# Kernel tuning notes

Hardware: AMD Instinct MI355X
Metric: run time of the kernel (lower is better)

## Reference

```python
import jax, jax.numpy as jnp
import numpy as np
import math

B, N, M, C, H = 4, 2048, 2048, 512, 4
D_V = C // H          # 128, used for scale and value head dim
D_QK = 2 * C // H     # 256, q/k head dim due to seq-axis split of the 2*dim qkv output
SCALE = D_V ** -0.5
EPS = 1e-12           # F.normalize eps


def _l2norm(t):
    n = jnp.linalg.norm(t, axis=-1, keepdims=True)
    return t / jnp.maximum(n, EPS)


def setup_inputs() -> dict:
    key = jax.random.key(0)
    k1, k2, k3, k4 = jax.random.split(key, 4)
    x = jax.random.normal(k1, (B, N, C), dtype=jnp.float32)
    context = jax.random.normal(k2, (B, M, C), dtype=jnp.float32)
    W_qkv = jax.random.normal(k3, (2 * C, C), dtype=jnp.float32) * 0.02  # torch Linear weight [out,in]
    W_proj = jax.random.normal(k4, (C, C), dtype=jnp.float32) * 0.02
    radius = jnp.ones((H,), dtype=jnp.float32) * math.sqrt(D_V)
    return {"x": x, "context": context, "W_qkv": W_qkv, "W_proj": W_proj, "radius": radius}


def reference(x, context, W_qkv, W_proj, radius):
    # qkv(cat([x, context], dim=1)) then split along sequence: q from x rows, k from context rows
    q = jnp.einsum('bnc,oc->bno', x, W_qkv)        # [B,N,2C]
    k = jnp.einsum('bmc,oc->bmo', context, W_qkv)  # [B,M,2C]
    q = q.reshape(B, N, H, D_QK).transpose(0, 2, 1, 3)       # [B,H,N,256]
    k = k.reshape(B, M, H, D_QK).transpose(0, 2, 1, 3)       # [B,H,M,256]
    v = context.reshape(B, M, H, D_V).transpose(0, 2, 1, 3)  # [B,H,M,128]
    r = radius[None, :, None, None]
    q = _l2norm(q) * r
    k = _l2norm(k) * r
    attn = jnp.einsum('bhnd,bhmd->bhnm', q, k) * SCALE
    attn = jax.nn.softmax(attn, axis=-1)
    out = jnp.einsum('bhnm,bhmd->bhnd', attn, v)
    out = out.transpose(0, 2, 1, 3).reshape(B, N, C)
    return jnp.einsum('bnc,oc->bno', out, W_proj)
```

## Files before the change

kernel.cpp:

```cpp
#include <hip/hip_runtime.h>
#include <hip/hip_bf16.h>
#include <stdint.h>

#define SCALE_F 0.08838834764831845f
#define LOG2E_F 1.4426950408889634f

typedef __attribute__((ext_vector_type(8))) short short8;
typedef __attribute__((ext_vector_type(4))) float f32x4;
typedef __attribute__((ext_vector_type(16))) float f32x16;
typedef __attribute__((ext_vector_type(2))) unsigned int uint2v;

__device__ __forceinline__ void g2l16(const void* g, void* l) {
  __builtin_amdgcn_global_load_lds(
      (const __attribute__((address_space(1))) void*)g,
      (__attribute__((address_space(3))) void*)l, 16, 0, 0);
}

__device__ __forceinline__ unsigned pkbf(float a, float b) {
  union { __hip_bfloat16 h[2]; unsigned u; } o;
  o.h[0] = __float2bfloat16(a); o.h[1] = __float2bfloat16(b);
  return o.u;
}

__global__ __launch_bounds__(256) void convert_all(
    const float* __restrict__ x, const float* __restrict__ wqkv,
    const float* __restrict__ wproj,
    __hip_bfloat16* __restrict__ ab, __hip_bfloat16* __restrict__ wb,
    __hip_bfloat16* __restrict__ wpb)
{
  size_t qi = (size_t)blockIdx.x * 256 + threadIdx.x;
  const float* src; __hip_bfloat16* dst; size_t off;
  if (qi < 1048576)      { src = x;     dst = ab;  off = qi; }
  else if (qi < 1179648) { src = wqkv;  dst = wb;  off = qi - 1048576; }
  else                   { src = wproj; dst = wpb; off = qi - 1179648; }
  float4 v = ((const float4*)src)[off];
  union { __hip_bfloat16 h4[4]; uint2 u; } o;
  o.h4[0] = __float2bfloat16(v.x); o.h4[1] = __float2bfloat16(v.y);
  o.h4[2] = __float2bfloat16(v.z); o.h4[3] = __float2bfloat16(v.w);
  ((uint2*)dst)[off] = o.u;
}

__global__ __launch_bounds__(256) void transpose_v(
    const float* __restrict__ ctx, __hip_bfloat16* __restrict__ vt,
    __hip_bfloat16* __restrict__ abctx)
{
  __shared__ float tile[128][33];
  const int bid = blockIdx.x;
  const int mt = bid & 63;
  const int bh = bid >> 6;
  const int h = bh & 3, b = bh >> 2;
  const int tid = threadIdx.x;
  for (int i = 0; i < 16; ++i) {
    int idx = i * 256 + tid;
    int mm = idx >> 7, d = idx & 127;
    tile[d][mm] = ctx[((size_t)b * 2048 + mt * 32 + mm) * 512 + h * 128 + d];
  }
  __syncthreads();
  for (int i = 0; i < 16; ++i) {
    int idx = i * 256 + tid;
    int d = idx >> 5, mm = idx & 31;
    vt[((size_t)bh * 128 + d) * 2048 + mt * 32 + mm] = __float2bfloat16(tile[d][mm]);
  }
  for (int i = 0; i < 16; ++i) {
    int idx = i * 256 + tid;
    int mm = idx >> 7, d = idx & 127;
    abctx[((size_t)b * 2048 + mt * 32 + mm) * 512 + h * 128 + d] =
        __float2bfloat16(tile[d][mm]);
  }
}

__global__ __launch_bounds__(256) void gemm_qkv(
    const __hip_bfloat16* __restrict__ A,
    const __hip_bfloat16* __restrict__ Bw,
    const float* __restrict__ radius,
    __hip_bfloat16* __restrict__ qn, __hip_bfloat16* __restrict__ kn)
{
  __shared__ __hip_bfloat16 sAB[384 * 32];
  __hip_bfloat16* sA = sAB;
  __hip_bfloat16* sB = sAB + 64 * 32;
  const int tid = threadIdx.x;
  const int wave = tid >> 6, lane = tid & 63;
  const int ln = lane & 15, q4 = lane >> 4;
  const int ro = blockIdx.x >> 2;
  const int co = blockIdx.x & 3;
  const __hip_bfloat16* Ab = A + (size_t)ro * 64 * 512;
  const __hip_bfloat16* Bb = Bw + (size_t)co * 256 * 512;
  const int row0 = tid >> 2, p0 = tid & 3;
  f32x4 acc[16] = {};
  for (int k0 = 0; k0 < 512; k0 += 32) {
    g2l16(Ab + (size_t)row0 * 512 + k0 + p0 * 8, (char*)sA + tid * 16);
#pragma unroll
    for (int i = 0; i < 4; ++i)
      g2l16(Bb + (size_t)(i * 64 + row0) * 512 + k0 + p0 * 8,
            (char*)sB + (i * 256 + tid) * 16);
    __syncthreads();
    short8 af = *(const short8*)(sA + (wave * 16 + ln) * 32 + q4 * 8);
#pragma unroll
    for (int ni = 0; ni < 16; ++ni) {
      short8 bf = *(const short8*)(sB + (ni * 16 + ln) * 32 + q4 * 8);
      acc[ni] = __builtin_amdgcn_mfma_f32_16x16x32_bf16(af, bf, acc[ni], 0, 0, 0);
    }
    __syncthreads();
  }
  const float rad = radius[co];
  const int grow0 = ro * 64;
  const bool isq = grow0 < 8192;
  const int rl = isq ? grow0 : grow0 - 8192;
  const float qfac = isq ? rad * rad * SCALE_F * LOG2E_F : 1.0f;
  float scl[4];
#pragma unroll
  for (int r = 0; r < 4; ++r) {
    float ss = 0.f;
#pragma unroll
    for (int ni = 0; ni < 16; ++ni) { float v = acc[ni][r]; ss += v * v; }
    ss += __shfl_xor(ss, 1); ss += __shfl_xor(ss, 2);
    ss += __shfl_xor(ss, 4); ss += __shfl_xor(ss, 8);
    scl[r] = qfac / fmaxf(sqrtf(ss), 1e-12f);
  }
  __hip_bfloat16* dstT = (isq ? qn : kn) +
      ((size_t)((rl >> 11) * 4 + co) * 2048 + (rl & 2047)) * 256;
  __hip_bfloat16* sEw = sAB + wave * 3072;
#pragma unroll
  for (int c = 0; c < 2; ++c) {
    if ((q4 >> 1) == c) {
      int lr = (q4 & 1) * 4;
#pragma unroll
      for (int r = 0; r < 4; ++r)
#pragma unroll
        for (int ni = 0; ni < 16; ++ni)
          sEw[(lr + r) * 264 + ni * 16 + ln] =
              __float2bfloat16(acc[ni][r] * scl[r]);
    }
    asm volatile("s_waitcnt lgkmcnt(0)" ::: "memory");
#pragma unroll
    for (int p = 0; p < 4; ++p) {
      int idx = p * 64 + lane;
      int rr = idx >> 5, c8 = idx & 31;
      short8 v = *(const short8*)(sEw + rr * 264 + c8 * 8);
      *(short8*)(dstT + (size_t)(wave * 16 + c * 8 + rr) * 256 + c8 * 8) = v;
    }
    asm volatile("s_waitcnt lgkmcnt(0)" ::: "memory");
  }
}

__global__ __launch_bounds__(256) void gemm_nt(
    const __hip_bfloat16* __restrict__ A, const __hip_bfloat16* __restrict__ B,
    float* __restrict__ C, int O, int K, int tiles_o)
{
  __shared__ __hip_bfloat16 sA[128 * 32];
  __shared__ __hip_bfloat16 sB[128 * 32];
  const int tid = threadIdx.x;
  const int wave = tid >> 6, lane = tid & 63;
  const int ln = lane & 15, q = lane >> 4;
  const int br = (blockIdx.x / tiles_o) * 128;
  const int bo = (blockIdx.x % tiles_o) * 128;
  const int wr = (wave >> 1) * 64, wc = (wave & 1) * 64;
  const __hip_bfloat16* Ab = A + (size_t)br * K;
  const __hip_bfloat16* Bb = B + (size_t)bo * K;
  const int row0 = tid >> 2, p0 = tid & 3;
  f32x4 acc[4][4] = {};
  for (int k0 = 0; k0 < K; k0 += 32) {
    for (int i = 0; i < 2; ++i) {
      int row = i * 64 + row0;
      g2l16(Ab + (size_t)row * K + k0 + p0 * 8, (char*)sA + (i * 256 + tid) * 16);
      g2l16(Bb + (size_t)row * K + k0 + p0 * 8, (char*)sB + (i * 256 + tid) * 16);
    }
    __syncthreads();
    short8 af[4], bfr[4];
    for (int mi = 0; mi < 4; ++mi)
      af[mi] = *(const short8*)(sA + (wr + mi * 16 + ln) * 32 + q * 8);
    for (int ni = 0; ni < 4; ++ni)
      bfr[ni] = *(const short8*)(sB + (wc + ni * 16 + ln) * 32 + q * 8);
    for (int mi = 0; mi < 4; ++mi)
      for (int ni = 0; ni < 4; ++ni)
        acc[mi][ni] = __builtin_amdgcn_mfma_f32_16x16x32_bf16(af[mi], bfr[ni], acc[mi][ni], 0, 0, 0);
    __syncthreads();
  }
  for (int mi = 0; mi < 4; ++mi)
    for (int ni = 0; ni < 4; ++ni) {
      int rg = br + wr + mi * 16 + q * 4;
      int cg = bo + wc + ni * 16 + ln;
      for (int r = 0; r < 4; ++r)
        C[(size_t)(rg + r) * O + cg] = acc[mi][ni][r];
    }
}

__global__ __launch_bounds__(256, 2) void attn(
    const __hip_bfloat16* __restrict__ qn,
    const __hip_bfloat16* __restrict__ kn,
    const __hip_bfloat16* __restrict__ vt,
    float* __restrict__ Op,
    float* __restrict__ den)
{
  __shared__ __hip_bfloat16 sK[2][32 * 256];
  __shared__ __hip_bfloat16 sV[2][128 * 32];
  const int tid = threadIdx.x, wave = tid >> 6, lane = tid & 63;
  const int m32 = lane & 31, hi = lane >> 5;
  const int i = blockIdx.x;
  const int bh = (i & 7) + 8 * ((i >> 3) & 1);
  const int half = (i >> 4) & 1;
  const int nt = i >> 5;
  const int mbase = half * 1024;
  const __hip_bfloat16* Q = qn + ((size_t)bh * 2048 + nt * 128 + wave * 32) * 256;
  const __hip_bfloat16* Kp = kn + (size_t)bh * 2048 * 256;
  const __hip_bfloat16* Vp = vt + (size_t)bh * 128 * 2048;

  short8 qf[16];
  for (int kk = 0; kk < 16; ++kk)
    qf[kk] = *(const short8*)(Q + m32 * 256 + kk * 16 + hi * 8);

  f32x16 oacc[4];
  for (int v = 0; v < 4; ++v)
    for (int j = 0; j < 16; ++j) oacc[v][j] = 0.f;
  float denom = 0.f;

  for (int t = 0; t < 4; ++t) {
    int D = t * 256 + tid, row = D >> 5, cc = D & 31;
    g2l16(Kp + (size_t)(mbase + row) * 256 + ((cc ^ (row & 7)) << 3),
          (char*)sK[0] + D * 16);
  }
  for (int t = 0; t < 2; ++t) {
    int D = t * 256 + tid, rd = D >> 2, cc = D & 3;
    g2l16(Vp + (size_t)rd * 2048 + mbase + ((cc ^ ((rd >> 1) & 3)) << 3),
          (char*)sV[0] + D * 16);
  }
  __syncthreads();

  for (int it = 0; it < 32; ++it) {
    const int cur = it & 1, nxt = cur ^ 1;
    if (it + 1 < 32) {
      const int m1 = mbase + (it + 1) * 32;
      for (int t = 0; t < 4; ++t) {
        int D = t * 256 + tid, row = D >> 5, cc = D & 31;
        g2l16(Kp + (size_t)(m1 + row) * 256 + ((cc ^ (row & 7)) << 3),
              (char*)sK[nxt] + D * 16);
      }
      for (int t = 0; t < 2; ++t) {
        int D = t * 256 + tid, rd = D >> 2, cc = D & 3;
        g2l16(Vp + (size_t)rd * 2048 + m1 + ((cc ^ ((rd >> 1) & 3)) << 3),
              (char*)sV[nxt] + D * 16);
      }
    }
    const __hip_bfloat16* sKc = sK[cur];
    f32x16 sa, sb;
    for (int j = 0; j < 16; ++j) { sa[j] = 0.f; sb[j] = 0.f; }
#pragma unroll
    for (int kk = 0; kk < 8; ++kk) {
      int ca = kk * 2 + hi, cb = (kk + 8) * 2 + hi;
      short8 kfa = *(const short8*)(sKc + m32 * 256 + ((ca ^ (m32 & 7)) << 3));
      short8 kfb = *(const short8*)(sKc + m32 * 256 + ((cb ^ (m32 & 7)) << 3));
      sa = __builtin_amdgcn_mfma_f32_32x32x16_bf16(kfa, qf[kk], sa, 0, 0, 0);
      sb = __builtin_amdgcn_mfma_f32_32x32x16_bf16(kfb, qf[kk + 8], sb, 0, 0, 0);
    }
    union { unsigned u[4]; short8 s; } ua, ub;
    {
      float e0, e1, e2, e3;
      unsigned u0, u1, u2, u3;
      e0 = __builtin_exp2f(sa[0] + sb[0]); e1 = __builtin_exp2f(sa[1] + sb[1]);
      e2 = __builtin_exp2f(sa[2] + sb[2]); e3 = __builtin_exp2f(sa[3] + sb[3]);
      denom += (e0 + e1) + (e2 + e3);
      u0 = pkbf(e0, e1); u1 = pkbf(e2, e3);
      e0 = __builtin_exp2f(sa[4] + sb[4]); e1 = __builtin_exp2f(sa[5] + sb[5]);
      e2 = __builtin_exp2f(sa[6] + sb[6]); e3 = __builtin_exp2f(sa[7] + sb[7]);
      denom += (e0 + e1) + (e2 + e3);
      u2 = pkbf(e0, e1); u3 = pkbf(e2, e3);
      uint2v s0 = __builtin_amdgcn_permlane32_swap(u0, u2, false, false);
      uint2v s1 = __builtin_amdgcn_permlane32_swap(u1, u3, false, false);
      ua.u[0] = s0.x; ua.u[1] = s1.x; ua.u[2] = s0.y; ua.u[3] = s1.y;
      e0 = __builtin_exp2f(sa[8] + sb[8]);   e1 = __builtin_exp2f(sa[9] + sb[9]);
      e2 = __builtin_exp2f(sa[10] + sb[10]); e3 = __builtin_exp2f(sa[11] + sb[11]);
      denom += (e0 + e1) + (e2 + e3);
      u0 = pkbf(e0, e1); u1 = pkbf(e2, e3);
      e0 = __builtin_exp2f(sa[12] + sb[12]); e1 = __builtin_exp2f(sa[13] + sb[13]);
      e2 = __builtin_exp2f(sa[14] + sb[14]); e3 = __builtin_exp2f(sa[15] + sb[15]);
      denom += (e0 + e1) + (e2 + e3);
      u2 = pkbf(e0, e1); u3 = pkbf(e2, e3);
      uint2v s2 = __builtin_amdgcn_permlane32_swap(u0, u2, false, false);
      uint2v s3 = __builtin_amdgcn_permlane32_swap(u1, u3, false, false);
      ub.u[0] = s2.x; ub.u[1] = s3.x; ub.u[2] = s2.y; ub.u[3] = s3.y;
    }
    const __hip_bfloat16* sVc = sV[cur];
#pragma unroll
    for (int kc = 0; kc < 2; ++kc) {
      short8 pf = kc ? ub.s : ua.s;
#pragma unroll
      for (int vi = 0; vi < 4; ++vi) {
        int rd = vi * 32 + m32;
        int c = kc * 2 + hi;
        short8 vf = *(const short8*)(sVc + rd * 32 + ((c ^ ((rd >> 1) & 3)) << 3));
        oacc[vi] = __builtin_amdgcn_mfma_f32_32x32x16_bf16(vf, pf, oacc[vi], 0, 0, 0);
      }
    }
    __syncthreads();
  }

  float dfull = denom + __shfl_xor(denom, 32);
  float* Opb = Op + (size_t)(half * 16 + bh) * 2048 * 128;
  float* denb = den + (size_t)(half * 16 + bh) * 2048;
  const int rbase = nt * 128 + wave * 32;
  if (hi == 0) denb[rbase + m32] = dfull;
  float* sc_ = (float*)(&sK[0][0]) + wave * 1056;
#pragma unroll
  for (int vi = 0; vi < 4; ++vi) {
#pragma unroll
    for (int reg = 0; reg < 16; ++reg) {
      int dL = (reg & 3) + 8 * (reg >> 2) + 4 * hi;
      sc_[m32 * 33 + dL] = oacc[vi][reg];
    }
    asm volatile("s_waitcnt lgkmcnt(0)" ::: "memory");
#pragma unroll
    for (int qq = 0; qq < 16; ++qq) {
      int qr = qq * 2 + hi;
      Opb[(size_t)(rbase + qr) * 128 + vi * 32 + m32] = sc_[qr * 33 + m32];
    }
    asm volatile("s_waitcnt lgkmcnt(0)" ::: "memory");
  }
}

__global__ __launch_bounds__(256) void combine(
    const float* __restrict__ Op, const float* __restrict__ den,
    __hip_bfloat16* __restrict__ ob)
{
  int qi = blockIdx.x * 256 + threadIdx.x;
  int r = qi >> 5;
  int dq = qi & 31;
  int bh = r >> 11, n = r & 2047, b = bh >> 2, h = bh & 3;
  float4 o0 = ((const float4*)Op)[qi];
  float4 o1 = ((const float4*)(Op + 4194304))[qi];
  float inv = 1.0f / (den[r] + den[32768 + r]);
  union { __hip_bfloat16 h4[4]; uint2 u; } o;
  o.h4[0] = __float2bfloat16((o0.x + o1.x) * inv);
  o.h4[1] = __float2bfloat16((o0.y + o1.y) * inv);
  o.h4[2] = __float2bfloat16((o0.z + o1.z) * inv);
  o.h4[3] = __float2bfloat16((o0.w + o1.w) * inv);
  *(uint2*)&ob[((size_t)b * 2048 + n) * 512 + h * 128 + dq * 4] = o.u;
}

extern "C" void kernel_launch(void* const* d_in, const int* in_sizes, int n_in,
                              void* d_out, int out_size, void* d_ws, size_t ws_size,
                              hipStream_t stream) {
  const float* x      = (const float*)d_in[0];
  const float* ctx    = (const float*)d_in[1];
  const float* wqkv   = (const float*)d_in[2];
  const float* wproj  = (const float*)d_in[3];
  const float* radius = (const float*)d_in[4];
  char* ws = (char*)d_ws;
  __hip_bfloat16* ab  = (__hip_bfloat16*)(ws);
  __hip_bfloat16* wb  = (__hip_bfloat16*)(ws + 16777216);
  __hip_bfloat16* wpb = (__hip_bfloat16*)(ws + 17825792);
  float*          Op  = (float*)(ws + 18350080);
  float*          den = (float*)(ws + 18350080 + 33554432);
  __hip_bfloat16* qn  = (__hip_bfloat16*)(ws + 85458944);
  __hip_bfloat16* kn  = (__hip_bfloat16*)(ws + 102236160);
  __hip_bfloat16* vt  = (__hip_bfloat16*)(ws + 119013376);
  __hip_bfloat16* ob  = (__hip_bfloat16*)(ws + 127401984);
  float* out = (float*)d_out;

  convert_all<<<4864, 256, 0, stream>>>(x, wqkv, wproj, ab, wb, wpb);
  transpose_v<<<1024, 256, 0, stream>>>(ctx, vt, ab + 4194304);
  gemm_qkv<<<1024, 256, 0, stream>>>(ab, wb, radius, qn, kn);
  attn<<<512, 256, 0, stream>>>(qn, kn, vt, Op, den);
  combine<<<4096, 256, 0, stream>>>(Op, den, ob);
  gemm_nt<<<256, 256, 0, stream>>>(ob, wpb, out, 512, 512, 4);
}
```

Before: 218.5 us.

## Retile QKV GEMM waves as 4x4 MFMA blocks and use raw exp2 in attention

The QKV projection GEMM changes its per-wave work split. Each wave used to own 16 rows across all 256 output columns; now it owns all 64 rows across a 64-column slice, computed as a 4x4 grid of MFMA fragments. This raises fragment reuse per LDS read (8 loads for 16 MFMAs instead of 17). Because a row's L2 norm now spans four waves, partial sums of squares go through shared memory with an extra block barrier, and the epilogue staging becomes block-wide with __syncthreads. Separately, the attention softmax replaces __builtin_exp2f with the raw hardware exp2 instruction, which drops any denormal/range handling wrappers.

Measured after the change: 214.3 us. About the same (-1.9%).

```diff
diff --git a/kernel.cpp b/kernel.cpp
--- a/kernel.cpp
+++ b/kernel.cpp
@@ -20,6 +20,14 @@
   union { __hip_bfloat16 h[2]; unsigned u; } o;
   o.h[0] = __float2bfloat16(a); o.h[1] = __float2bfloat16(b);
   return o.u;
+}
+
+__device__ __forceinline__ float fexp2(float x) {
+#if __has_builtin(__builtin_amdgcn_exp2f)
+  return __builtin_amdgcn_exp2f(x);
+#else
+  float r; asm("v_exp_f32 %0, %1" : "=v"(r) : "v"(x)); return r;
+#endif
 }
 
 __global__ __launch_bounds__(256) void convert_all(
@@ -75,7 +83,8 @@
     const float* __restrict__ radius,
     __hip_bfloat16* __restrict__ qn, __hip_bfloat16* __restrict__ kn)
 {
-  __shared__ __hip_bfloat16 sAB[384 * 32];
+  __shared__ __hip_bfloat16 sAB[320 * 32];
+  __shared__ float sNorm[4][64];
   __hip_bfloat16* sA = sAB;
   __hip_bfloat16* sB = sAB + 64 * 32;
   const int tid = threadIdx.x;
@@ -86,7 +95,7 @@
   const __hip_bfloat16* Ab = A + (size_t)ro * 64 * 512;
   const __hip_bfloat16* Bb = Bw + (size_t)co * 256 * 512;
   const int row0 = tid >> 2, p0 = tid & 3;
-  f32x4 acc[16] = {};
+  f32x4 acc[4][4] = {};
   for (int k0 = 0; k0 < 512; k0 += 32) {
     g2l16(Ab + (size_t)row0 * 512 + k0 + p0 * 8, (char*)sA + tid * 16);
 #pragma unroll
@@ -94,12 +103,18 @@
       g2l16(Bb + (size_t)(i * 64 + row0) * 512 + k0 + p0 * 8,
             (char*)sB + (i * 256 + tid) * 16);
     __syncthreads();
-    short8 af = *(const short8*)(sA + (wave * 16 + ln) * 32 + q4 * 8);
-#pragma unroll
-    for (int ni = 0; ni < 16; ++ni) {
-      short8 bf = *(const short8*)(sB + (ni * 16 + ln) * 32 + q4 * 8);
-      acc[ni] = __builtin_amdgcn_mfma_f32_16x16x32_bf16(af, bf, acc[ni], 0, 0, 0);
-    }
+    short8 af[4], bfr[4];
+#pragma unroll
+    for (int mi = 0; mi < 4; ++mi)
+      af[mi] = *(const short8*)(sA + (mi * 16 + ln) * 32 + q4 * 8);
+#pragma unroll
+    for (int ni = 0; ni < 4; ++ni)
+      bfr[ni] = *(const short8*)(sB + (wave * 64 + ni * 16 + ln) * 32 + q4 * 8);
+#pragma unroll
+    for (int mi = 0; mi < 4; ++mi)
+#pragma unroll
+      for (int ni = 0; ni < 4; ++ni)
+        acc[mi][ni] = __builtin_amdgcn_mfma_f32_16x16x32_bf16(af[mi], bfr[ni], acc[mi][ni], 0, 0, 0);
     __syncthreads();
   }
   const float rad = radius[co];
@@ -107,39 +122,52 @@
   const bool isq = grow0 < 8192;
   const int rl = isq ? grow0 : grow0 - 8192;
   const float qfac = isq ? rad * rad * SCALE_F * LOG2E_F : 1.0f;
-  float scl[4];
-#pragma unroll
-  for (int r = 0; r < 4; ++r) {
-    float ss = 0.f;
-#pragma unroll
-    for (int ni = 0; ni < 16; ++ni) { float v = acc[ni][r]; ss += v * v; }
-    ss += __shfl_xor(ss, 1); ss += __shfl_xor(ss, 2);
-    ss += __shfl_xor(ss, 4); ss += __shfl_xor(ss, 8);
-    scl[r] = qfac / fmaxf(sqrtf(ss), 1e-12f);
-  }
+#pragma unroll
+  for (int mi = 0; mi < 4; ++mi)
+#pragma unroll
+    for (int r = 0; r < 4; ++r) {
+      float ss = acc[mi][0][r] * acc[mi][0][r] + acc[mi][1][r] * acc[mi][1][r]
+               + acc[mi][2][r] * acc[mi][2][r] + acc[mi][3][r] * acc[mi][3][r];
+      ss += __shfl_xor(ss, 1); ss += __shfl_xor(ss, 2);
+      ss += __shfl_xor(ss, 4); ss += __shfl_xor(ss, 8);
+      if (ln == 0) sNorm[wave][mi * 16 + q4 * 4 + r] = ss;
+    }
+  __syncthreads();
+  float scl[4][4];
+#pragma unroll
+  for (int mi = 0; mi < 4; ++mi)
+#pragma unroll
+    for (int r = 0; r < 4; ++r) {
+      int row = mi * 16 + q4 * 4 + r;
+      float tot = sNorm[0][row] + sNorm[1][row] + sNorm[2][row] + sNorm[3][row];
+      scl[mi][r] = qfac / fmaxf(sqrtf(tot), 1e-12f);
+    }
   __hip_bfloat16* dstT = (isq ? qn : kn) +
       ((size_t)((rl >> 11) * 4 + co) * 2048 + (rl & 2047)) * 256;
-  __hip_bfloat16* sEw = sAB + wave * 3072;
+  __hip_bfloat16* sE = sAB;
 #pragma unroll
   for (int c = 0; c < 2; ++c) {
-    if ((q4 >> 1) == c) {
-      int lr = (q4 & 1) * 4;
-#pragma unroll
-      for (int r = 0; r < 4; ++r)
-#pragma unroll
-        for (int ni = 0; ni < 16; ++ni)
-          sEw[(lr + r) * 264 + ni * 16 + ln] =
-              __float2bfloat16(acc[ni][r] * scl[r]);
-    }
-    asm volatile("s_waitcnt lgkmcnt(0)" ::: "memory");
+#pragma unroll
+    for (int mi2 = 0; mi2 < 2; ++mi2) {
+      int mi = c * 2 + mi2;
+#pragma unroll
+      for (int r = 0; r < 4; ++r) {
+        int lr = mi2 * 16 + q4 * 4 + r;
+#pragma unroll
+        for (int ni = 0; ni < 4; ++ni)
+          sE[lr * 264 + wave * 64 + ni * 16 + ln] =
+              __float2bfloat16(acc[mi][ni][r] * scl[mi][r]);
+      }
+    }
+    __syncthreads();
 #pragma unroll
     for (int p = 0; p < 4; ++p) {
-      int idx = p * 64 + lane;
+      int idx = p * 256 + tid;
       int rr = idx >> 5, c8 = idx & 31;
-      short8 v = *(const short8*)(sEw + rr * 264 + c8 * 8);
-      *(short8*)(dstT + (size_t)(wave * 16 + c * 8 + rr) * 256 + c8 * 8) = v;
-    }
-    asm volatile("s_waitcnt lgkmcnt(0)" ::: "memory");
+      short8 v = *(const short8*)(sE + rr * 264 + c8 * 8);
+      *(short8*)(dstT + (size_t)(c * 32 + rr) * 256 + c8 * 8) = v;
+    }
+    __syncthreads();
   }
 }
 
@@ -256,23 +284,23 @@
     {
       float e0, e1, e2, e3;
       unsigned u0, u1, u2, u3;
-      e0 = __builtin_exp2f(sa[0] + sb[0]); e1 = __builtin_exp2f(sa[1] + sb[1]);
-      e2 = __builtin_exp2f(sa[2] + sb[2]); e3 = __builtin_exp2f(sa[3] + sb[3]);
+      e0 = fexp2(sa[0] + sb[0]); e1 = fexp2(sa[1] + sb[1]);
+      e2 = fexp2(sa[2] + sb[2]); e3 = fexp2(sa[3] + sb[3]);
       denom += (e0 + e1) + (e2 + e3);
       u0 = pkbf(e0, e1); u1 = pkbf(e2, e3);
-      e0 = __builtin_exp2f(sa[4] + sb[4]); e1 = __builtin_exp2f(sa[5] + sb[5]);
-      e2 = __builtin_exp2f(sa[6] + sb[6]); e3 = __builtin_exp2f(sa[7] + sb[7]);
+      e0 = fexp2(sa[4] + sb[4]); e1 = fexp2(sa[5] + sb[5]);
+      e2 = fexp2(sa[6] + sb[6]); e3 = fexp2(sa[7] + sb[7]);
       denom += (e0 + e1) + (e2 + e3);
       u2 = pkbf(e0, e1); u3 = pkbf(e2, e3);
       uint2v s0 = __builtin_amdgcn_permlane32_swap(u0, u2, false, false);
       uint2v s1 = __builtin_amdgcn_permlane32_swap(u1, u3, false, false);
       ua.u[0] = s0.x; ua.u[1] = s1.x; ua.u[2] = s0.y; ua.u[3] = s1.y;
-      e0 = __builtin_exp2f(sa[8] + sb[8]);   e1 = __builtin_exp2f(sa[9] + sb[9]);
-      e2 = __builtin_exp2f(sa[10] + sb[10]); e3 = __builtin_exp2f(sa[11] + sb[11]);
+      e0 = fexp2(sa[8] + sb[8]);   e1 = fexp2(sa[9] + sb[9]);
+      e2 = fexp2(sa[10] + sb[10]); e3 = fexp2(sa[11] + sb[11]);
       denom += (e0 + e1) + (e2 + e3);
       u0 = pkbf(e0, e1); u1 = pkbf(e2, e3);
-      e0 = __builtin_exp2f(sa[12] + sb[12]); e1 = __builtin_exp2f(sa[13] + sb[13]);
-      e2 = __builtin_exp2f(sa[14] + sb[14]); e3 = __builtin_exp2f(sa[15] + sb[15]);
+      e0 = fexp2(sa[12] + sb[12]); e1 = fexp2(sa[13] + sb[13]);
+      e2 = fexp2(sa[14] + sb[14]); e3 = fexp2(sa[15] + sb[15]);
       denom += (e0 + e1) + (e2 + e3);
       u2 = pkbf(e0, e1); u3 = pkbf(e2, e3);
       uint2v s2 = __builtin_amdgcn_permlane32_swap(u0, u2, false, false);
```
